# Performance work log

Measured on AMD Instinct MI355X. Metric: run time of the kernel, lower is better.

The kernel has to match this reference:

```python
import jax, jax.numpy as jnp
import numpy as np
from jax import lax

KERNEL = 3
EPS = 0.01


def _box_sum(x, k):
    # sum over kxk window, stride 1, SAME-style explicit padding of k//2
    pad = k // 2
    return lax.reduce_window(
        x, 0.0, lax.add,
        window_dimensions=(1, 1, k, k),
        window_strides=(1, 1, 1, 1),
        padding=((0, 0), (0, 0), (pad, pad), (pad, pad)),
    )


def _box_counts(h, w, k, dtype):
    # number of valid (non-padded) elements in each window (count_include_pad=False)
    ones = jnp.ones((1, 1, h, w), dtype=dtype)
    return _box_sum(ones, k)


def _blur(x, counts, k):
    return _box_sum(x, k) / counts


def setup_inputs() -> dict:
    key = jax.random.key(0)
    k1, k2 = jax.random.split(key)
    shape = (8, 16, 512, 512)
    inp = jax.random.normal(k1, shape, dtype=jnp.float32)
    guide = jax.random.normal(k2, shape, dtype=jnp.float32)
    return {"input": inp, "guide": guide}


def reference(input, guide):
    I, p = input, guide
    B, C, H, W = I.shape
    counts = _box_counts(H, W, KERNEL, I.dtype)  # [1,1,H,W]

    mean_I = _blur(I, counts, KERNEL)
    mean_p = _blur(p, counts, KERNEL)
    mean_II = _blur(I * I, counts, KERNEL)
    mean_Ip = _blur(I * p, counts, KERNEL)

    var_I = mean_II - mean_I * mean_I
    cov_Ip = mean_Ip - mean_I * mean_p

    a = cov_Ip / (var_I + EPS)
    b = mean_p - a * mean_I

    mean_a = _blur(a, counts, KERNEL)
    mean_b = _blur(b, counts, KERNEL)

    return mean_a * I + mean_b
```

## Files before the change

### kernel.cpp

```cpp
#include <hip/hip_runtime.h>


constexpr int W  = 512;
constexpr int H  = 512;
constexpr int TW = 64;
constexpr int TH = 16;
constexpr int IW = TW + 4;
constexpr int IH = TH + 4;
constexpr int AW = TW + 2;
constexpr int AH = TH + 2;
constexpr float EPS = 0.01f;

__global__ __launch_bounds__(256) void guide_filter_kernel(
    const float* __restrict__ I, const float* __restrict__ P,
    float* __restrict__ O)
{
    __shared__ float sI[IH][IW];
    __shared__ float sP[IH][IW];
    __shared__ float sA[AH][AW];
    __shared__ float sB[AH][AW];

    const int tid = threadIdx.x;
    const int x0  = blockIdx.x * TW;
    const int y0  = blockIdx.y * TH;
    const size_t img_off = (size_t)blockIdx.z * (size_t)(W * H);
    const float* Ibase = I + img_off;
    const float* Pbase = P + img_off;
    float*       Obase = (float*)O + img_off;

    for (int idx = tid; idx < IW * IH; idx += 256) {
        const int iy = idx / IW;
        const int ix = idx - iy * IW;
        const int gx = x0 - 2 + ix;
        const int gy = y0 - 2 + iy;
        float vi = 0.0f, vp = 0.0f;
        if (gx >= 0 && gx < W && gy >= 0 && gy < H) {
            const int g = gy * W + gx;
            vi = Ibase[g];
            vp = Pbase[g];
        }
        sI[iy][ix] = vi;
        sP[iy][ix] = vp;
    }
    __syncthreads();

    for (int idx = tid; idx < AW * AH; idx += 256) {
        const int ay  = idx / AW;
        const int ax  = idx - ay * AW;
        const int agx = x0 - 1 + ax;
        const int agy = y0 - 1 + ay;
        float a = 0.0f, b = 0.0f;
        if (agx >= 0 && agx < W && agy >= 0 && agy < H) {
            float sIs = 0.f, sPs = 0.f, sII = 0.f, sIP = 0.f;
            #pragma unroll
            for (int dy = 0; dy < 3; ++dy) {
                #pragma unroll
                for (int dx = 0; dx < 3; ++dx) {
                    const float vi = sI[ay + dy][ax + dx];
                    const float vp = sP[ay + dy][ax + dx];
                    sIs += vi;
                    sPs += vp;
                    sII = fmaf(vi, vi, sII);
                    sIP = fmaf(vi, vp, sIP);
                }
            }
            const int cx = min(agx + 1, W - 1) - max(agx - 1, 0) + 1;
            const int cy = min(agy + 1, H - 1) - max(agy - 1, 0) + 1;
            const float inv = __builtin_amdgcn_rcpf((float)(cx * cy));
            const float mI  = sIs * inv;
            const float mP  = sPs * inv;
            const float varI = fmaf(-mI, mI, sII * inv);
            const float cov  = fmaf(-mI, mP, sIP * inv);
            a = cov * __builtin_amdgcn_rcpf(varI + EPS);
            b = fmaf(-a, mI, mP);
        }
        sA[ay][ax] = a;
        sB[ay][ax] = b;
    }
    __syncthreads();

    for (int idx = tid; idx < TW * TH; idx += 256) {
        const int oy = idx >> 6;
        const int ox = idx & 63;
        const int gx = x0 + ox;
        const int gy = y0 + oy;
        float sa = 0.f, sb = 0.f;
        #pragma unroll
        for (int dy = 0; dy < 3; ++dy) {
            #pragma unroll
            for (int dx = 0; dx < 3; ++dx) {
                sa += sA[oy + dy][ox + dx];
                sb += sB[oy + dy][ox + dx];
            }
        }
        const int cx = min(gx + 1, W - 1) - max(gx - 1, 0) + 1;
        const int cy = min(gy + 1, H - 1) - max(gy - 1, 0) + 1;
        const float inv = __builtin_amdgcn_rcpf((float)(cx * cy));
        const float ma = sa * inv;
        const float mb = sb * inv;
        Obase[gy * W + gx] = fmaf(ma, sI[oy + 2][ox + 2], mb);
    }
}

extern "C" void kernel_launch(void* const* d_in, const int* in_sizes, int n_in,
                              void* d_out, int out_size, void* d_ws, size_t ws_size,
                              hipStream_t stream) {
    const float* I = (const float*)d_in[0];
    const float* P = (const float*)d_in[1];
    float*       O = (float*)d_out;
    const int images = in_sizes[0] / (W * H);
    dim3 grid(W / TW, H / TH, images);
    guide_filter_kernel<<<grid, dim3(256), 0, stream>>>(I, P, O);
}
```

Measured before the change: 349.3 us.

## Interleave I/P in shared memory and compute box sums per vertical strip

Stores I and P interleaved as float2 in shared memory, loaded with float2 global reads and float4 shared writes, and packs a and b into one float2 array. The first stencil stage now has 198 threads each compute a 6-row strip, reusing vertical neighbours in registers instead of reloading nine taps per output. The second stage gives each thread 4 output rows so horizontal sums are shared across rows. This cuts shared-memory traffic and redundant adds, but only 198 of 256 threads do work in stage two, and register pressure goes up.

```diff
diff --git a/kernel.cpp b/kernel.cpp
--- a/kernel.cpp
+++ b/kernel.cpp
@@ -15,10 +15,8 @@
     const float* __restrict__ I, const float* __restrict__ P,
     float* __restrict__ O)
 {
-    __shared__ float sI[IH][IW];
-    __shared__ float sP[IH][IW];
-    __shared__ float sA[AH][AW];
-    __shared__ float sB[AH][AW];
+    __shared__ __align__(16) float2 sIP[IH][IW];
+    __shared__ float2 sAB[AH][AW];
 
     const int tid = threadIdx.x;
     const int x0  = blockIdx.x * TW;
@@ -28,77 +26,108 @@
     const float* Pbase = P + img_off;
     float*       Obase = (float*)O + img_off;
 
-    for (int idx = tid; idx < IW * IH; idx += 256) {
-        const int iy = idx / IW;
-        const int ix = idx - iy * IW;
-        const int gx = x0 - 2 + ix;
-        const int gy = y0 - 2 + iy;
-        float vi = 0.0f, vp = 0.0f;
-        if (gx >= 0 && gx < W && gy >= 0 && gy < H) {
+    for (int t = tid; t < 34 * IH; t += 256) {
+        const int row = t / 34;
+        const int cp  = t - row * 34;
+        const int gy  = y0 - 2 + row;
+        const int gx  = x0 - 2 + 2 * cp;
+        float i0 = 0.f, i1 = 0.f, p0 = 0.f, p1 = 0.f;
+        if (gy >= 0 && gy < H) {
             const int g = gy * W + gx;
-            vi = Ibase[g];
-            vp = Pbase[g];
+            if (gx >= 0 && gx + 1 < W) {
+                const float2 vi = *(const float2*)(Ibase + g);
+                const float2 vp = *(const float2*)(Pbase + g);
+                i0 = vi.x; i1 = vi.y; p0 = vp.x; p1 = vp.y;
+            } else {
+                if (gx >= 0 && gx < W)         { i0 = Ibase[g];     p0 = Pbase[g]; }
+                if (gx + 1 >= 0 && gx + 1 < W) { i1 = Ibase[g + 1]; p1 = Pbase[g + 1]; }
+            }
         }
-        sI[iy][ix] = vi;
-        sP[iy][ix] = vp;
+        *(float4*)&sIP[row][2 * cp] = make_float4(i0, p0, i1, p1);
     }
     __syncthreads();
 
-    for (int idx = tid; idx < AW * AH; idx += 256) {
-        const int ay  = idx / AW;
-        const int ax  = idx - ay * AW;
-        const int agx = x0 - 1 + ax;
-        const int agy = y0 - 1 + ay;
-        float a = 0.0f, b = 0.0f;
-        if (agx >= 0 && agx < W && agy >= 0 && agy < H) {
-            float sIs = 0.f, sPs = 0.f, sII = 0.f, sIP = 0.f;
+    if (tid < 3 * AW) {
+        const int strip = tid / AW;
+        const int ax    = tid - strip * AW;
+        const int ay0   = strip * 6;
+
+        float wI[6], wP[6], wII[6], wIP[6];
+        #pragma unroll
+        for (int j = 0; j < 6; ++j) { wI[j] = wP[j] = wII[j] = wIP[j] = 0.f; }
+
+        #pragma unroll
+        for (int c = 0; c < 3; ++c) {
+            float2 v[8];
             #pragma unroll
-            for (int dy = 0; dy < 3; ++dy) {
-                #pragma unroll
-                for (int dx = 0; dx < 3; ++dx) {
-                    const float vi = sI[ay + dy][ax + dx];
-                    const float vp = sP[ay + dy][ax + dx];
-                    sIs += vi;
-                    sPs += vp;
-                    sII = fmaf(vi, vi, sII);
-                    sIP = fmaf(vi, vp, sIP);
-                }
+            for (int j = 0; j < 8; ++j) v[j] = sIP[ay0 + j][ax + c];
+            float ii[8], ip[8];
+            #pragma unroll
+            for (int j = 0; j < 8; ++j) {
+                ii[j] = v[j].x * v[j].x;
+                ip[j] = v[j].x * v[j].y;
             }
-            const int cx = min(agx + 1, W - 1) - max(agx - 1, 0) + 1;
-            const int cy = min(agy + 1, H - 1) - max(agy - 1, 0) + 1;
-            const float inv = __builtin_amdgcn_rcpf((float)(cx * cy));
-            const float mI  = sIs * inv;
-            const float mP  = sPs * inv;
-            const float varI = fmaf(-mI, mI, sII * inv);
-            const float cov  = fmaf(-mI, mP, sIP * inv);
-            a = cov * __builtin_amdgcn_rcpf(varI + EPS);
-            b = fmaf(-a, mI, mP);
+            #pragma unroll
+            for (int j = 0; j < 6; ++j) {
+                wI[j]  += v[j].x  + v[j + 1].x  + v[j + 2].x;
+                wP[j]  += v[j].y  + v[j + 1].y  + v[j + 2].y;
+                wII[j] += ii[j]   + ii[j + 1]   + ii[j + 2];
+                wIP[j] += ip[j]   + ip[j + 1]   + ip[j + 2];
+            }
         }
-        sA[ay][ax] = a;
-        sB[ay][ax] = b;
+
+        const int gx = x0 - 1 + ax;
+        const bool xok = (gx >= 0) & (gx < W);
+        const float cx = 3.f - (float)(gx == 0) - (float)(gx == W - 1);
+        #pragma unroll
+        for (int j = 0; j < 6; ++j) {
+            const int ay = ay0 + j;
+            const int gy = y0 - 1 + ay;
+            float a = 0.f, b = 0.f;
+            if (xok & (gy >= 0) & (gy < H)) {
+                const float cy  = 3.f - (float)(gy == 0) - (float)(gy == H - 1);
+                const float inv = __builtin_amdgcn_rcpf(cx * cy);
+                const float mI   = wI[j] * inv;
+                const float mP   = wP[j] * inv;
+                const float varI = fmaf(-mI, mI, wII[j] * inv);
+                const float cov  = fmaf(-mI, mP, wIP[j] * inv);
+                a = cov * __builtin_amdgcn_rcpf(varI + EPS);
+                b = fmaf(-a, mI, mP);
+            }
+            sAB[ay][ax] = make_float2(a, b);
+        }
     }
     __syncthreads();
 
-    for (int idx = tid; idx < TW * TH; idx += 256) {
-        const int oy = idx >> 6;
-        const int ox = idx & 63;
-        const int gx = x0 + ox;
-        const int gy = y0 + oy;
-        float sa = 0.f, sb = 0.f;
+    {
+        const int x  = tid & 63;
+        const int r0 = (tid >> 6) * 4;
+        float2 ab[6][3];
         #pragma unroll
-        for (int dy = 0; dy < 3; ++dy) {
+        for (int j = 0; j < 6; ++j)
             #pragma unroll
-            for (int dx = 0; dx < 3; ++dx) {
-                sa += sA[oy + dy][ox + dx];
-                sb += sB[oy + dy][ox + dx];
-            }
+            for (int c = 0; c < 3; ++c)
+                ab[j][c] = sAB[r0 + j][x + c];
+
+        float hA[6], hB[6];
+        #pragma unroll
+        for (int j = 0; j < 6; ++j) {
+            hA[j] = ab[j][0].x + ab[j][1].x + ab[j][2].x;
+            hB[j] = ab[j][0].y + ab[j][1].y + ab[j][2].y;
         }
-        const int cx = min(gx + 1, W - 1) - max(gx - 1, 0) + 1;
-        const int cy = min(gy + 1, H - 1) - max(gy - 1, 0) + 1;
-        const float inv = __builtin_amdgcn_rcpf((float)(cx * cy));
-        const float ma = sa * inv;
-        const float mb = sb * inv;
-        Obase[gy * W + gx] = fmaf(ma, sI[oy + 2][ox + 2], mb);
+
+        const int gx = x0 + x;
+        const float cx = 3.f - (float)(gx == 0) - (float)(gx == W - 1);
+        #pragma unroll
+        for (int j = 0; j < 4; ++j) {
+            const int gy = y0 + r0 + j;
+            const float cy  = 3.f - (float)(gy == 0) - (float)(gy == H - 1);
+            const float inv = __builtin_amdgcn_rcpf(cx * cy);
+            const float ma  = (hA[j] + hA[j + 1] + hA[j + 2]) * inv;
+            const float mb  = (hB[j] + hB[j + 1] + hB[j + 2]) * inv;
+            const float Ic  = sIP[r0 + j + 2][x + 2].x;
+            Obase[gy * W + gx] = fmaf(ma, Ic, mb);
+        }
     }
 }
 
```

After: 332.2 us. -4.9%, faster.
